# Kernel optimization log

Hardware: AMD Instinct MI355X
Metric: run time of the kernel (lower is better)

## Reference

```python
import jax, jax.numpy as jnp
import numpy as np

# Mesh sampling: out[m] = sum_k vals[m,k] * x[cols[m,k]]  (3 nnz per row, barycentric)
B, N, C = 8, 50000, 128   # batch, input vertices, channels
M, K = 25000, 3           # output vertices, nnz per row


def setup_inputs() -> dict:
    key = jax.random.key(0)
    k1, k2, k3 = jax.random.split(key, 3)
    x = jax.random.normal(k1, (B, N, C), dtype=jnp.float32)
    cols = jax.random.randint(k2, (M, K), 0, N, dtype=jnp.int32)
    v = jax.random.uniform(k3, (M, K), dtype=jnp.float32)
    vals = v / jnp.sum(v, axis=-1, keepdims=True)  # barycentric-like weights
    return {"x": x, "cols": cols, "vals": vals}


def reference(x, cols, vals):
    # Equivalent to torch.sparse.mm(S, x.permute(1,0,2).flatten(1)) reshaped back:
    # out[b, m, c] = sum_k vals[m, k] * x[b, cols[m, k], c]
    gathered = x[:, cols, :]                      # [B, M, K, C]
    return jnp.einsum('mk,bmkc->bmc', vals, gathered)  # [B, M, C]
```

## Files before the change

### kernel.cpp

```cpp
#include <hip/hip_runtime.h>


#define B_ 8
#define N_ 50000
#define C_ 128
#define M_ 25000

__global__ __launch_bounds__(256) void mesh_gather_kernel(
    const float* __restrict__ x,
    const int* __restrict__ cols,
    const float* __restrict__ vals,
    float* __restrict__ out)
{
    int t = blockIdx.x * blockDim.x + threadIdx.x;
    const int total = B_ * M_ * (C_ / 4);
    if (t >= total) return;

    int c4 = t & 31;
    int m  = (t >> 5) % M_;
    int b  = t / (M_ * 32);

    int i0 = cols[m * 3 + 0];
    int i1 = cols[m * 3 + 1];
    int i2 = cols[m * 3 + 2];
    float v0 = vals[m * 3 + 0];
    float v1 = vals[m * 3 + 1];
    float v2 = vals[m * 3 + 2];

    const float4* xb = (const float4*)(x + (long long)b * N_ * C_);
    float4 a = xb[(long long)i0 * 32 + c4];
    float4 bq = xb[(long long)i1 * 32 + c4];
    float4 cq = xb[(long long)i2 * 32 + c4];

    float4 r;
    r.x = v0 * a.x + v1 * bq.x + v2 * cq.x;
    r.y = v0 * a.y + v1 * bq.y + v2 * cq.y;
    r.z = v0 * a.z + v1 * bq.z + v2 * cq.z;
    r.w = v0 * a.w + v1 * bq.w + v2 * cq.w;

    ((float4*)out)[t] = r;
}

extern "C" void kernel_launch(void* const* d_in, const int* in_sizes, int n_in,
                              void* d_out, int out_size, void* d_ws, size_t ws_size,
                              hipStream_t stream) {
    const float* x    = (const float*)d_in[0];
    const int*   cols = (const int*)d_in[1];
    const float* vals = (const float*)d_in[2];
    float* out = (float*)d_out;

    const int total = B_ * M_ * (C_ / 4);
    const int block = 256;
    const int grid = (total + block - 1) / block;
    mesh_gather_kernel<<<grid, block, 0, stream>>>(x, cols, vals, out);
}
```

Measured before the change: 305.2 us.

## Transpose x to vertex-major layout before gathering all batches per row

Adds a pre-pass that rewrites x into a [N,B,C] workspace so each gathered vertex is one contiguous 4KB row covering all batches. The gather kernel then handles 8 output rows per block with all 8 batches per thread-block. This aims to improve the efficiency of the random gathers, at the cost of an extra full read and write of x every call. It falls back to the original kernel when the workspace is too small.

```diff
diff --git a/kernel.cpp b/kernel.cpp
--- a/kernel.cpp
+++ b/kernel.cpp
@@ -5,8 +5,55 @@
 #define N_ 50000
 #define C_ 128
 #define M_ 25000
+#define GPM 8
 
-__global__ __launch_bounds__(256) void mesh_gather_kernel(
+__global__ __launch_bounds__(256) void transpose_kernel(
+    const float* __restrict__ x, float* __restrict__ xt)
+{
+    int n = blockIdx.x;
+    int t = threadIdx.x;
+    int b = t >> 5, c4 = t & 31;
+    float4 v = ((const float4*)x)[((long long)b * N_ + n) * 32 + c4];
+    ((float4*)xt)[(long long)n * 256 + t] = v;
+}
+
+__global__ __launch_bounds__(256) void gather_kernel(
+    const float* __restrict__ xt,
+    const int* __restrict__ cols,
+    const float* __restrict__ vals,
+    float* __restrict__ out)
+{
+    int m0 = blockIdx.x * GPM;
+    int t = threadIdx.x;
+    int b = t >> 5, c4 = t & 31;
+    const float4* xt4 = (const float4*)xt;
+    float4* out4 = (float4*)out;
+
+    #pragma unroll 2
+    for (int j = 0; j < GPM; ++j) {
+        int m = m0 + j;
+        int i0 = cols[m * 3 + 0];
+        int i1 = cols[m * 3 + 1];
+        int i2 = cols[m * 3 + 2];
+        float v0 = vals[m * 3 + 0];
+        float v1 = vals[m * 3 + 1];
+        float v2 = vals[m * 3 + 2];
+
+        float4 a = xt4[(long long)i0 * 256 + t];
+        float4 q = xt4[(long long)i1 * 256 + t];
+        float4 w = xt4[(long long)i2 * 256 + t];
+
+        float4 r;
+        r.x = v0 * a.x + v1 * q.x + v2 * w.x;
+        r.y = v0 * a.y + v1 * q.y + v2 * w.y;
+        r.z = v0 * a.z + v1 * q.z + v2 * w.z;
+        r.w = v0 * a.w + v1 * q.w + v2 * w.w;
+
+        out4[((long long)b * M_ + m) * 32 + c4] = r;
+    }
+}
+
+__global__ __launch_bounds__(256) void mesh_gather_direct(
     const float* __restrict__ x,
     const int* __restrict__ cols,
     const float* __restrict__ vals,
@@ -29,14 +76,14 @@
 
     const float4* xb = (const float4*)(x + (long long)b * N_ * C_);
     float4 a = xb[(long long)i0 * 32 + c4];
-    float4 bq = xb[(long long)i1 * 32 + c4];
-    float4 cq = xb[(long long)i2 * 32 + c4];
+    float4 q = xb[(long long)i1 * 32 + c4];
+    float4 w = xb[(long long)i2 * 32 + c4];
 
     float4 r;
-    r.x = v0 * a.x + v1 * bq.x + v2 * cq.x;
-    r.y = v0 * a.y + v1 * bq.y + v2 * cq.y;
-    r.z = v0 * a.z + v1 * bq.z + v2 * cq.z;
-    r.w = v0 * a.w + v1 * bq.w + v2 * cq.w;
+    r.x = v0 * a.x + v1 * q.x + v2 * w.x;
+    r.y = v0 * a.y + v1 * q.y + v2 * w.y;
+    r.z = v0 * a.z + v1 * q.z + v2 * w.z;
+    r.w = v0 * a.w + v1 * q.w + v2 * w.w;
 
     ((float4*)out)[t] = r;
 }
@@ -49,8 +96,14 @@
     const float* vals = (const float*)d_in[2];
     float* out = (float*)d_out;
 
-    const int total = B_ * M_ * (C_ / 4);
-    const int block = 256;
-    const int grid = (total + block - 1) / block;
-    mesh_gather_kernel<<<grid, block, 0, stream>>>(x, cols, vals, out);
+    const size_t xt_bytes = (size_t)N_ * B_ * C_ * sizeof(float);
+
+    if (ws_size >= xt_bytes) {
+        float* xt = (float*)d_ws;
+        transpose_kernel<<<N_, 256, 0, stream>>>(x, xt);
+        gather_kernel<<<M_ / GPM, 256, 0, stream>>>(xt, cols, vals, out);
+    } else {
+        const int total = B_ * M_ * (C_ / 4);
+        mesh_gather_direct<<<(total + 255) / 256, 256, 0, stream>>>(x, cols, vals, out);
+    }
 }
```

After: 376.6 us. +23.4%, slower.
